# Optimization experiments

Measured on AMD Instinct MI355X. Metric: run time of the kernel, lower is better.

The kernel has to match this reference:

```python
import jax, jax.numpy as jnp
import numpy as np

STRIDES = (8, 16, 32, 64, 128)
LEVEL_HW = ((128, 160), (64, 80), (32, 40), (16, 20), (8, 10))
IMG_H, IMG_W = 1024, 1280
B, NUM_CLASSES = 16, 20
SCORE_THR, IOU_THR, MAX_DET = 0.05, 0.6, 1000


def _coords_all():
    # coords_fmap2orig for every level, concatenated -> [N, 2] (x, y)
    cs = []
    for (h, w), s in zip(LEVEL_HW, STRIDES):
        sx = jnp.arange(w, dtype=jnp.float32) * s + s // 2
        sy = jnp.arange(h, dtype=jnp.float32) * s + s // 2
        yy, xx = jnp.meshgrid(sy, sx, indexing='ij')
        cs.append(jnp.stack([xx.reshape(-1), yy.reshape(-1)], -1))
    return jnp.concatenate(cs, 0)


def _reshape_cat(levels):
    # list of [B,C,h,w] -> [B, sum(h*w), C]
    return jnp.concatenate(
        [p.transpose(0, 2, 3, 1).reshape(p.shape[0], -1, p.shape[1]) for p in levels], 1)


def _decode(cls_l, cnt_l, reg_l, coords):
    cls = jax.nn.sigmoid(_reshape_cat(cls_l))           # [B,N,C]
    cnt = jax.nn.sigmoid(_reshape_cat(cnt_l))[..., 0]   # [B,N]
    reg = _reshape_cat(reg_l)                           # [B,N,4] ltrb
    scores = jnp.sqrt(jnp.max(cls, -1) * cnt)           # add_centerness + sqrt
    classes = jnp.argmax(cls, -1) + 1
    boxes = jnp.concatenate([coords[None] - reg[..., :2], coords[None] + reg[..., 2:]], -1)
    return scores, classes, boxes


def _nms_keep(boxes, scores, classes, valid):
    # masked greedy per-class NMS on fixed size M; returns keep mask [M]
    boxes = jax.lax.stop_gradient(boxes)
    scores = jax.lax.stop_gradient(scores)
    maxc = jnp.max(jnp.where(valid[:, None], boxes, 0.0))
    b = boxes + (classes.astype(boxes.dtype) * (maxc + 1.0))[:, None]  # class offsets
    order = jnp.argsort(-jnp.where(valid, scores, -jnp.inf))
    b = b[order]
    v = valid[order]
    x1, y1, x2, y2 = b[:, 0], b[:, 1], b[:, 2], b[:, 3]
    areas = (x2 - x1 + 1.0) * (y2 - y1 + 1.0)
    iw = jnp.clip(jnp.minimum(x2[:, None], x2[None, :]) - jnp.maximum(x1[:, None], x1[None, :]) + 1.0, 0.0)
    ih = jnp.clip(jnp.minimum(y2[:, None], y2[None, :]) - jnp.maximum(y1[:, None], y1[None, :]) + 1.0, 0.0)
    inter = iw * ih
    iou = inter / (areas[:, None] + areas[None, :] - inter)
    M = boxes.shape[0]

    def body(i, carry):
        keep, sup = carry
        k = v[i] & (~sup[i])
        keep = keep.at[i].set(k)
        sup = sup | (k & (iou[i] > IOU_THR))
        return keep, sup

    keep_s, _ = jax.lax.fori_loop(0, M, body, (jnp.zeros(M, bool), jnp.zeros(M, bool)))
    return jnp.zeros(M, bool).at[order].set(keep_s)


def _forward(args):
    cls_r, cnt_r, reg_r = args[0:5], args[5:10], args[10:15]
    cls_i, cnt_i, reg_i = args[15:20], args[20:25], args[25:30]
    coords = _coords_all()
    s_r, c_r, b_r = _decode(cls_r, cnt_r, reg_r, coords)
    s_i, c_i, b_i = _decode(cls_i, cnt_i, reg_i, coords)
    scores = jnp.concatenate([s_r, s_i], 1)   # [B, 2N]
    classes = jnp.concatenate([c_r, c_i], 1)
    boxes = jnp.concatenate([b_r, b_i], 1)
    top_s, top_i = jax.lax.top_k(scores, MAX_DET)
    top_c = jnp.take_along_axis(classes, top_i, 1)
    top_b = jnp.take_along_axis(boxes, top_i[..., None], 1)
    valid = top_s >= SCORE_THR
    keep = jax.vmap(_nms_keep)(top_b, top_s, top_c, valid)
    # ClipBoxes: clamp to image bounds
    top_b = jnp.maximum(top_b, 0.0)
    xs = jnp.minimum(top_b[..., 0::2], IMG_W - 1.0)
    ys = jnp.minimum(top_b[..., 1::2], IMG_H - 1.0)
    top_b = jnp.stack([xs[..., 0], ys[..., 0], xs[..., 1], ys[..., 1]], -1)
    kf = keep.astype(top_s.dtype)
    return top_s * kf, top_c * keep, top_b * kf[..., None], keep


def setup_inputs() -> dict:
    key = jax.random.key(0)
    chans = {'cls': NUM_CLASSES, 'cnt': 1, 'reg': 4}
    inp = {}
    i = 0
    for mod in ('r', 'i'):
        for kind in ('cls', 'cnt', 'reg'):
            for l, (h, w) in enumerate(LEVEL_HW):
                k = jax.random.fold_in(key, i); i += 1
                inp[f'{kind}_{mod}_{l}'] = jax.random.normal(k, (B, chans[kind], h, w), jnp.float32)
    return inp


def reference(cls_r_0, cls_r_1, cls_r_2, cls_r_3, cls_r_4,
              cnt_r_0, cnt_r_1, cnt_r_2, cnt_r_3, cnt_r_4,
              reg_r_0, reg_r_1, reg_r_2, reg_r_3, reg_r_4,
              cls_i_0, cls_i_1, cls_i_2, cls_i_3, cls_i_4,
              cnt_i_0, cnt_i_1, cnt_i_2, cnt_i_3, cnt_i_4,
              reg_i_0, reg_i_1, reg_i_2, reg_i_3, reg_i_4):
    args = [cls_r_0, cls_r_1, cls_r_2, cls_r_3, cls_r_4,
            cnt_r_0, cnt_r_1, cnt_r_2, cnt_r_3, cnt_r_4,
            reg_r_0, reg_r_1, reg_r_2, reg_r_3, reg_r_4,
            cls_i_0, cls_i_1, cls_i_2, cls_i_3, cls_i_4,
            cnt_i_0, cnt_i_1, cnt_i_2, cnt_i_3, cnt_i_4,
            reg_i_0, reg_i_1, reg_i_2, reg_i_3, reg_i_4]
    return _forward(args)
```

## Files before the change

### kernel.cpp

```cpp
#include <hip/hip_runtime.h>
#include <hip/hip_bf16.h>

typedef unsigned long long u64;
typedef unsigned int u32;

#define NTOT    54560
#define NMOD    27280
#define BATCH   16
#define KPAD    1024
#define MAXD    1000
#define NBIN    16384
#define CAND    6144

struct Ptrs { const float* p[30]; };

constexpr size_t SZ_KEY   = (size_t)BATCH * NTOT * 8;
constexpr size_t SZ_TOPK  = (size_t)BATCH * KPAD * 8;
constexpr size_t SZ_TRAW  = (size_t)BATCH * KPAD * 16;
constexpr size_t SZ_T1    = (size_t)BATCH * KPAD * 4;
constexpr size_t SZ_MAXC  = (size_t)BATCH * 32 * 4;
constexpr size_t SZ_VALID = (size_t)BATCH * 32 * 4;
constexpr size_t SZ_MASK  = (size_t)BATCH * KPAD * 32 * 4;

constexpr size_t OFF_KEY    = 0;
constexpr size_t OFF_TOPK   = OFF_KEY   + SZ_KEY;
constexpr size_t OFF_TRAW   = OFF_TOPK  + SZ_TOPK;
constexpr size_t OFF_TSCORE = OFF_TRAW  + SZ_TRAW;
constexpr size_t OFF_TCLSF  = OFF_TSCORE+ SZ_T1;
constexpr size_t OFF_MAXC   = OFF_TCLSF + SZ_T1;
constexpr size_t OFF_VALID  = OFF_MAXC  + SZ_MAXC;
constexpr size_t OFF_MASK   = OFF_VALID + SZ_VALID;

__device__ inline void level_of(int nm, int& l, int& pos, int& w, int& s, int& hw) {
    if (nm < 20480)      { l = 0; pos = nm;         w = 160; s = 8;   hw = 20480; }
    else if (nm < 25600) { l = 1; pos = nm - 20480; w = 80;  s = 16;  hw = 5120; }
    else if (nm < 26880) { l = 2; pos = nm - 25600; w = 40;  s = 32;  hw = 1280; }
    else if (nm < 27200) { l = 3; pos = nm - 26880; w = 20;  s = 64;  hw = 320; }
    else                 { l = 4; pos = nm - 27200; w = 10;  s = 128; hw = 80; }
}

__device__ inline float sigm(float x) { return 1.0f / (1.0f + expf(-x)); }

__device__ inline void ld_lds16(const float* g, float* l) {
    __builtin_amdgcn_global_load_lds(
        (const __attribute__((address_space(1))) void*)g,
        (__attribute__((address_space(3))) void*)l, 16, 0, 0);
}

__global__ __launch_bounds__(128)
void decode_kernel(Ptrs ptrs, u64* __restrict__ keyAll) {
    __shared__ float lds[21 * 512];
    int cc = blockIdx.x;
    int b = blockIdx.y;

    if (cc >= 100) {
        int t = (cc - 100) * 128 + threadIdx.x;
        if (t >= 3360) return;
        int mod = t / 1680;
        int tm = t % 1680;
        int q = t & 3;
        int nm = 25600 + (tm & ~3);
        int l, pos, w, s, hw;
        level_of(nm, l, pos, w, s, hw);
        (void)w; (void)s;
        const float* clsP = ptrs.p[mod * 15 + l];
        const float* cntP = ptrs.p[mod * 15 + 5 + l];
        const float4* cb = (const float4*)(clsP + (size_t)b * 20 * hw + pos);
        int hw4 = hw >> 2;
        int c0 = q * 5;
        float4 v[5];
        #pragma unroll
        for (int c = 0; c < 5; ++c) v[c] = cb[(size_t)(c0 + c) * hw4];
        float4 cv = *(const float4*)(cntP + (size_t)b * hw + pos);
        float4 mx = v[0];
        #pragma unroll
        for (int c = 1; c < 5; ++c) {
            mx.x = fmaxf(mx.x, v[c].x); mx.y = fmaxf(mx.y, v[c].y);
            mx.z = fmaxf(mx.z, v[c].z); mx.w = fmaxf(mx.w, v[c].w);
        }
        mx.x = fmaxf(mx.x, __shfl_xor(mx.x, 1));
        mx.y = fmaxf(mx.y, __shfl_xor(mx.y, 1));
        mx.z = fmaxf(mx.z, __shfl_xor(mx.z, 1));
        mx.w = fmaxf(mx.w, __shfl_xor(mx.w, 1));
        mx.x = fmaxf(mx.x, __shfl_xor(mx.x, 2));
        mx.y = fmaxf(mx.y, __shfl_xor(mx.y, 2));
        mx.z = fmaxf(mx.z, __shfl_xor(mx.z, 2));
        mx.w = fmaxf(mx.w, __shfl_xor(mx.w, 2));
        float ma = (q & 1) ? ((q & 2) ? mx.w : mx.y) : ((q & 2) ? mx.z : mx.x);
        float ca = (q & 1) ? ((q & 2) ? cv.w : cv.y) : ((q & 2) ? cv.z : cv.x);
        u32 sb = __float_as_uint(sqrtf(__fmul_rn(sigm(ma), sigm(ca))));
        int n = mod * NMOD + nm + q;
        keyAll[(size_t)b * NTOT + n] = ((u64)sb << 16) | (u64)(65535 - n);
        return;
    }

    int mod = cc / 50, c = cc % 50;
    int l     = (c < 40) ? 0 : 1;
    int hw    = (c < 40) ? 20480 : 5120;
    int pos0  = (c < 40) ? c * 512 : (c - 40) * 512;
    int nmb   = (l == 0) ? pos0 : 20480 + pos0;
    const float* clsP = ptrs.p[mod * 15 + l];
    const float* cntP = ptrs.p[mod * 15 + 5 + l];
    int wave = threadIdx.x >> 6, lane = threadIdx.x & 63;

    const float* cbase = clsP + (size_t)b * 20 * hw + pos0 + wave * 256 + lane * 4;
    float* dbase = lds + wave * 256;
    #pragma unroll
    for (int ch = 0; ch < 20; ++ch)
        ld_lds16(cbase + (size_t)ch * hw, dbase + ch * 512);
    ld_lds16(cntP + (size_t)b * hw + pos0 + wave * 256 + lane * 4, dbase + 20 * 512);
    __syncthreads();

    int t = threadIdx.x;
    const float4* l4 = (const float4*)lds;
    float4 mx = l4[t];
    #pragma unroll
    for (int ch = 1; ch < 20; ++ch) {
        float4 v = l4[ch * 128 + t];
        mx.x = fmaxf(mx.x, v.x); mx.y = fmaxf(mx.y, v.y);
        mx.z = fmaxf(mx.z, v.z); mx.w = fmaxf(mx.w, v.w);
    }
    float4 cv = l4[20 * 128 + t];

    int n = mod * NMOD + nmb + t * 4;
    u32 s0 = __float_as_uint(sqrtf(__fmul_rn(sigm(mx.x), sigm(cv.x))));
    u32 s1 = __float_as_uint(sqrtf(__fmul_rn(sigm(mx.y), sigm(cv.y))));
    u32 s2 = __float_as_uint(sqrtf(__fmul_rn(sigm(mx.z), sigm(cv.z))));
    u32 s3 = __float_as_uint(sqrtf(__fmul_rn(sigm(mx.w), sigm(cv.w))));
    ulonglong2* ka2 = (ulonglong2*)(keyAll + (size_t)b * NTOT + n);
    ulonglong2 k01, k23;
    k01.x = ((u64)s0 << 16) | (u64)(65535 - n);
    k01.y = ((u64)s1 << 16) | (u64)(65535 - (n + 1));
    k23.x = ((u64)s2 << 16) | (u64)(65535 - (n + 2));
    k23.y = ((u64)s3 << 16) | (u64)(65535 - (n + 3));
    ka2[0] = k01; ka2[1] = k23;
}

__global__ __launch_bounds__(1024)
void select_kernel(const u64* __restrict__ keyAll, u64* __restrict__ topkey,
                   u32* __restrict__ maxcG) {
    int b = blockIdx.x, tid = threadIdx.x;
    int lane = tid & 63, wid = tid >> 6;
    __shared__ u32 shist[NBIN];
    __shared__ u64 scand[CAND];
    __shared__ u64 stopk[KPAD];
    __shared__ u32 warep[16];
    __shared__ int sB1;

    if (tid == 0) maxcG[b * 32] = 0u;
    #pragma unroll
    for (int j = 0; j < NBIN / 1024; ++j) shist[tid + j * 1024] = 0u;
    __syncthreads();

    const u64* keys = keyAll + (size_t)b * NTOT;
    const u64 SENT = ~0ull;
    for (int n0 = 0; n0 < NTOT; n0 += 8192) {
        u64 kk[8];
        #pragma unroll
        for (int r = 0; r < 8; ++r) {
            int idx = n0 + r * 1024 + tid;
            kk[r] = (idx < NTOT) ? keys[idx] : SENT;
        }
        #pragma unroll
        for (int r = 0; r < 8; ++r)
            if (kk[r] != SENT) atomicAdd(&shist[(u32)(kk[r] >> 32)], 1u);
    }
    __syncthreads();

    u32 loc[16]; u32 sum = 0;
    #pragma unroll
    for (int j = 0; j < 16; ++j) { loc[j] = shist[NBIN - 1 - (tid * 16 + j)]; sum += loc[j]; }
    u32 v = sum;
    #pragma unroll
    for (int off = 1; off < 64; off <<= 1) {
        u32 t2 = (u32)__shfl_up((int)v, off);
        if (lane >= off) v += t2;
    }
    if (lane == 63) warep[wid] = v;
    __syncthreads();
    if (tid < 16) {
        u32 p = warep[tid];
        #pragma unroll
        for (int off = 1; off < 16; off <<= 1) {
            u32 t2 = (u32)__shfl_up((int)p, off);
            if (tid >= off) p += t2;
        }
        warep[tid] = p;
    }
    __syncthreads();
    u32 incl = v + (wid ? warep[wid - 1] : 0u);
    u32 excl = incl - sum;
    if (excl < (u32)MAXD && incl >= (u32)MAXD) {
        u32 c = excl;
        #pragma unroll
        for (int j = 0; j < 16; ++j) {
            c += loc[j];
            if (c >= (u32)MAXD) { sB1 = NBIN - 1 - (tid * 16 + j); break; }
        }
    }
    u32 run = excl;
    #pragma unroll
    for (int j = 0; j < 16; ++j) {
        int bin = NBIN - 1 - (tid * 16 + j);
        shist[bin] = run;
        run += loc[j];
    }
    __syncthreads();
    int B1 = sB1;

    for (int n0 = 0; n0 < NTOT; n0 += 8192) {
        u64 kk[8];
        #pragma unroll
        for (int r = 0; r < 8; ++r) {
            int idx = n0 + r * 1024 + tid;
            kk[r] = (idx < NTOT) ? keys[idx] : 0ull;
        }
        #pragma unroll
        for (int r = 0; r < 8; ++r) {
            if (kk[r] != 0ull && (int)(kk[r] >> 32) >= B1) {
                u32 p = atomicAdd(&shist[(u32)(kk[r] >> 32)], 1u);
                if (p < CAND) scand[p] = kk[r];
            }
        }
    }
    __syncthreads();
    int Ctot = min((int)shist[B1], CAND);

    for (int i = tid; i < Ctot; i += 1024) {
        u64 ki = scand[i];
        int bin = (int)(ki >> 32);
        int st = (int)shist[bin + 1];
        int en = min((int)shist[bin], Ctot);
        int pos = st;
        for (int j = st; j < en; ++j) pos += (scand[j] > ki) ? 1 : 0;
        if (pos < MAXD) stopk[pos] = ki;
    }
    __syncthreads();
    if (tid < MAXD) topkey[(size_t)b * KPAD + tid] = stopk[tid];
}

__global__ __launch_bounds__(128)
void gather_kernel(Ptrs ptrs, const u64* __restrict__ topkey,
                   float4* __restrict__ traw, float* __restrict__ tscore,
                   float* __restrict__ tclsf, u32* __restrict__ validwords,
                   u32* __restrict__ maxcG) {
    #pragma clang fp contract(off)
    int b = blockIdx.y;
    int tid = threadIdx.x;
    int half = tid & 1;
    int i = blockIdx.x * 64 + (tid >> 1);
    int active = (i < MAXD);

    float score = 0.f;
    float best = -1.0f; int bi = 0;
    float ra = 0.f, rb2 = 0.f;
    int pos = 0, w = 1, s = 0;
    if (active) {
        u64 key = topkey[(size_t)b * KPAD + i];
        int n = 65535 - (int)(key & 0xFFFFull);
        score = __uint_as_float((u32)(key >> 16));
        int mod = (n >= NMOD) ? 1 : 0;
        int nm = n - mod * NMOD;
        int l, hw;
        level_of(nm, l, pos, w, s, hw);
        const float* clsP = ptrs.p[mod * 15 + l];
        const float* regP = ptrs.p[mod * 15 + 10 + l];
        const float* cbp = clsP + (size_t)b * 20 * hw + pos;
        const float* rbp = regP + (size_t)b * 4 * hw + pos;
        float cl[10];
        int c0 = half * 10;
        #pragma unroll
        for (int c = 0; c < 10; ++c) cl[c] = cbp[(size_t)(c0 + c) * hw];
        ra  = rbp[(size_t)(half * 2) * hw];
        rb2 = rbp[(size_t)(half * 2 + 1) * hw];
        #pragma unroll
        for (int c = 0; c < 10; ++c) {
            float p = sigm(cl[c]);
            if (p > best) { best = p; bi = c0 + c; }
        }
    }
    float po  = __shfl_xor(best, 1);
    int   bio = __shfl_xor(bi, 1);
    float rao = __shfl_xor(ra, 1);
    float rbo = __shfl_xor(rb2, 1);
    if (half == 0) { if (po > best)  { best = po; bi = bio; } }
    else           { if (po >= best) { best = po; bi = bio; } }
    float clsf = active ? (float)(bi + 1) : 0.f;
    float r0 = half ? rao : ra,  r1 = half ? rbo : rb2;
    float r2 = half ? ra  : rao, r3 = half ? rb2 : rbo;

    float4 bx = make_float4(0.f, 0.f, 0.f, 0.f);
    if (active) {
        int xi = pos % w, yi = pos / w;
        float cx = (float)(xi * s + (s >> 1));
        float cy = (float)(yi * s + (s >> 1));
        bx.x = cx - r0; bx.y = cy - r1; bx.z = cx + r2; bx.w = cy + r3;
    }
    int valid = active && (score >= 0.05f) && (half == 0);
    float contrib = valid ? fmaxf(0.0f, fmaxf(fmaxf(bx.x, bx.y), fmaxf(bx.z, bx.w))) : 0.0f;
    float red = contrib;
    #pragma unroll
    for (int off = 32; off > 0; off >>= 1) red = fmaxf(red, __shfl_down(red, off));
    if ((tid & 63) == 0) atomicMax(&maxcG[b * 32], __float_as_uint(red));
    u64 ball = __ballot(valid != 0);
    if ((tid & 63) == 0) {
        u32 word = 0;
        for (int j = 0; j < 32; ++j) word |= (u32)((ball >> (2 * j)) & 1ull) << j;
        validwords[b * 32 + blockIdx.x * 2 + (tid >> 6)] = word;
    }
    if (half == 0) {
        size_t oo = (size_t)b * KPAD + i;
        traw[oo] = bx; tscore[oo] = score; tclsf[oo] = clsf;
    }
}

#define SW(t) ((((t) & 31) << 3) | ((t) >> 5))
__global__ __launch_bounds__(256)
void mask_kernel(const float4* __restrict__ traw, const float* __restrict__ tclsf,
                 const u32* __restrict__ maxcG, u32* __restrict__ maskG) {
    #pragma clang fp contract(off)
    int u = blockIdx.x, b = blockIdx.y, tid = threadIdx.x;
    int g, wg;
    if (u < 32)      { g = u >> 2;              wg = u & 3; }
    else if (u < 56) { int d = u - 32; g = 8  + d / 3;        wg = 1 + d % 3; }
    else if (u < 72) { int d = u - 56; g = 16 + (d >> 1);     wg = 2 + (d & 1); }
    else             { g = 24 + (u - 72);       wg = 3; }
    int i0 = g * 32, j0 = wg * 256;
    float m1 = __uint_as_float(maxcG[b * 32]) + 1.0f;

    __shared__ float cx1[256], cy1[256], cx2[256], cy2[256], ca[256];
    {
        int t = tid;
        float4 f = traw[(size_t)b * KPAD + j0 + t];
        float o = __fmul_rn(tclsf[(size_t)b * KPAD + j0 + t], m1);
        float ox1 = __fadd_rn(f.x, o), oy1 = __fadd_rn(f.y, o);
        float ox2 = __fadd_rn(f.z, o), oy2 = __fadd_rn(f.w, o);
        float dw = ox2 - ox1 + 1.0f;
        float dh = oy2 - oy1 + 1.0f;
        int ts = SW(t);
        cx1[ts] = ox1; cy1[ts] = oy1; cx2[ts] = ox2; cy2[ts] = oy2;
        ca[ts] = __fmul_rn(dw, dh);
    }
    __syncthreads();

    int ir = tid >> 3, wr = tid & 7;
    int i = i0 + ir;
    float4 fi = traw[(size_t)b * KPAD + i];
    float oi = __fmul_rn(tclsf[(size_t)b * KPAD + i], m1);
    float ix1 = __fadd_rn(fi.x, oi), iy1 = __fadd_rn(fi.y, oi);
    float ix2 = __fadd_rn(fi.z, oi), iy2 = __fadd_rn(fi.w, oi);
    float dwi = ix2 - ix1 + 1.0f, dhi = iy2 - iy1 + 1.0f;
    float ai = __fmul_rn(dwi, dhi);
    u32 bits = 0;
    int jb = wr * 32;
    for (int jj = 0; jj < 32; ++jj) {
        int js = SW(jb + jj);
        float iw = fminf(ix2, cx2[js]) - fmaxf(ix1, cx1[js]) + 1.0f;
        iw = fmaxf(iw, 0.0f);
        float ih = fminf(iy2, cy2[js]) - fmaxf(iy1, cy1[js]) + 1.0f;
        ih = fmaxf(ih, 0.0f);
        float inter = iw * ih;
        float denom = (ai + ca[js]) - inter;
        float iou = inter / denom;
        bits |= (iou > 0.6f) ? (1u << jj) : 0u;
    }
    maskG[((size_t)b * KPAD + i) * 32 + wg * 8 + wr] = bits;
}

__global__ __launch_bounds__(512)
void scan_out_kernel(const u32* __restrict__ maskG, const u32* __restrict__ validbits,
                     const float4* __restrict__ traw, const float* __restrict__ tscore,
                     const float* __restrict__ tclsf, float* __restrict__ out) {
    __shared__ u32 sm[KPAD * 32];
    __shared__ u32 keeps[32];
    int b = blockIdx.x, tid = threadIdx.x;

    const uint4* s4 = (const uint4*)(maskG + (size_t)b * KPAD * 32);
    uint4* d4 = (uint4*)sm;
    #pragma unroll
    for (int r = 0; r < 16; ++r) {
        int w4 = tid + r * 512;
        int row = w4 >> 3, c4 = w4 & 7;
        d4[(row << 3) | (c4 ^ (row & 7))] = s4[w4];
    }
    __syncthreads();

    if (tid < 64) {
        int lane = tid, lw = lane & 31;
        int rbase = (lane >> 5) << 4;
        u32 vword = validbits[b * 32 + lw];
        u32 removed = 0u, keepw = 0u;
        for (int g = 0; g < 32; ++g) {
            int i0 = g << 5;
            u32 intra = sm[((i0 + lw) << 5) | (g ^ ((lw & 7) << 2))];
            u32 remg = (u32)__builtin_amdgcn_readlane((int)removed, g);
            u32 valg = (u32)__builtin_amdgcn_readlane((int)vword, g);
            u32 cand = valg & ~remg;
            u32 keep32 = 0u, sup = 0u;
            #pragma unroll
            for (int i = 0; i < 32; ++i) {
                u32 mi = (u32)__builtin_amdgcn_readlane((int)intra, i);
                u32 kb = cand & ~sup & (1u << i);
                sup |= kb ? mi : 0u;
                keep32 |= kb;
            }
            u32 ksh = keep32 >> rbase;
            u32 acc0 = 0u, acc1 = 0u;
            #pragma unroll
            for (int r = 0; r < 16; r += 2) {
                u32 r0 = sm[((i0 + rbase + r)     << 5) | (lw ^ ((r & 7) << 2))];
                u32 r1 = sm[((i0 + rbase + r + 1) << 5) | (lw ^ (((r + 1) & 7) << 2))];
                acc0 |= ((ksh >> r) & 1u)       ? r0 : 0u;
                acc1 |= ((ksh >> (r + 1)) & 1u) ? r1 : 0u;
            }
            u32 acc = acc0 | acc1;
            acc |= (u32)__shfl_xor((int)acc, 32);
            removed |= acc;
            if (lw == g) keepw = keep32;
        }
        if (lane < 32) keeps[lw] = keepw;
    }
    __syncthreads();

    const int BQ = BATCH * MAXD;
    for (int s2 = tid; s2 < MAXD; s2 += 512) {
        u32 kf = (keeps[s2 >> 5] >> (s2 & 31)) & 1u;
        size_t oo = (size_t)b * KPAD + s2;
        float score = tscore[oo];
        float clsf = tclsf[oo];
        float4 bx = traw[oo];
        float x1 = fminf(fmaxf(bx.x, 0.f), 1279.f);
        float y1 = fminf(fmaxf(bx.y, 0.f), 1023.f);
        float x2 = fminf(fmaxf(bx.z, 0.f), 1279.f);
        float y2 = fminf(fmaxf(bx.w, 0.f), 1023.f);
        int base = b * MAXD + s2;
        out[base] = kf ? score : 0.0f;
        out[BQ + base] = kf ? clsf : 0.0f;
        float* ob = out + 2 * BQ + (size_t)base * 4;
        ob[0] = kf ? x1 : 0.f; ob[1] = kf ? y1 : 0.f;
        ob[2] = kf ? x2 : 0.f; ob[3] = kf ? y2 : 0.f;
        out[6 * BQ + base] = kf ? 1.0f : 0.0f;
    }
}

extern "C" void kernel_launch(void* const* d_in, const int* in_sizes, int n_in,
                              void* d_out, int out_size, void* d_ws, size_t ws_size,
                              hipStream_t stream) {
    Ptrs ptrs;
    for (int i = 0; i < 30; ++i) ptrs.p[i] = (const float*)d_in[i];

    char* ws = (char*)d_ws;
    u64*    keyAll    = (u64*)   (ws + OFF_KEY);
    u64*    topkey    = (u64*)   (ws + OFF_TOPK);
    float4* traw      = (float4*)(ws + OFF_TRAW);
    float*  tscore    = (float*) (ws + OFF_TSCORE);
    float*  tclsf     = (float*) (ws + OFF_TCLSF);
    u32*    maxcG     = (u32*)   (ws + OFF_MAXC);
    u32*    validbits = (u32*)   (ws + OFF_VALID);
    u32*    maskG     = (u32*)   (ws + OFF_MASK);
    float*  out       = (float*)d_out;

    decode_kernel<<<dim3(127, BATCH), 128, 0, stream>>>(ptrs, keyAll);
    select_kernel<<<BATCH, 1024, 0, stream>>>(keyAll, topkey, maxcG);
    gather_kernel<<<dim3(16, BATCH), 128, 0, stream>>>(ptrs, topkey, traw, tscore, tclsf,
                                                       validbits, maxcG);
    mask_kernel<<<dim3(80, BATCH), 256, 0, stream>>>(traw, tclsf, maxcG, maskG);
    scan_out_kernel<<<BATCH, 512, 0, stream>>>(maskG, validbits, traw, tscore, tclsf, out);
}
```

Measured before the change: 236.3 us.

## Split top-k select into global histogram, scan, scatter and fixup kernels

The single-block-per-image select kernel is replaced by a pipeline. The histogram is built with global atomics inside the decode kernel, which removes one full pass over the keys. A scan kernel then finds the threshold bin, a multi-block scatter kernel writes candidates to global memory, and a fixup kernel ranks them in LDS. This spreads the select work over more CUs than the old 16 blocks. The cost is contended global atomics, extra kernel launches and a zeroing kernel.

```diff
diff --git a/kernel.cpp b/kernel.cpp
--- a/kernel.cpp
+++ b/kernel.cpp
@@ -21,6 +21,9 @@
 constexpr size_t SZ_MAXC  = (size_t)BATCH * 32 * 4;
 constexpr size_t SZ_VALID = (size_t)BATCH * 32 * 4;
 constexpr size_t SZ_MASK  = (size_t)BATCH * KPAD * 32 * 4;
+constexpr size_t SZ_GHIST = (size_t)BATCH * NBIN * 4;
+constexpr size_t SZ_GB1   = 256;
+constexpr size_t SZ_GCAND = (size_t)BATCH * CAND * 8;
 
 constexpr size_t OFF_KEY    = 0;
 constexpr size_t OFF_TOPK   = OFF_KEY   + SZ_KEY;
@@ -30,6 +33,9 @@
 constexpr size_t OFF_MAXC   = OFF_TCLSF + SZ_T1;
 constexpr size_t OFF_VALID  = OFF_MAXC  + SZ_MAXC;
 constexpr size_t OFF_MASK   = OFF_VALID + SZ_VALID;
+constexpr size_t OFF_GHIST  = OFF_MASK  + SZ_MASK;
+constexpr size_t OFF_GB1    = OFF_GHIST + SZ_GHIST;
+constexpr size_t OFF_GCAND  = OFF_GB1   + SZ_GB1;
 
 __device__ inline void level_of(int nm, int& l, int& pos, int& w, int& s, int& hw) {
     if (nm < 20480)      { l = 0; pos = nm;         w = 160; s = 8;   hw = 20480; }
@@ -47,11 +53,19 @@
         (__attribute__((address_space(3))) void*)l, 16, 0, 0);
 }
 
+__global__ __launch_bounds__(256)
+void init_kernel(uint4* __restrict__ ghist4, u32* __restrict__ maxcG) {
+    int i = blockIdx.x * 256 + threadIdx.x;
+    ghist4[i] = make_uint4(0u, 0u, 0u, 0u);
+    if (i < BATCH) maxcG[i * 32] = 0u;
+}
+
 __global__ __launch_bounds__(128)
-void decode_kernel(Ptrs ptrs, u64* __restrict__ keyAll) {
+void decode_kernel(Ptrs ptrs, u64* __restrict__ keyAll, u32* __restrict__ ghist) {
     __shared__ float lds[21 * 512];
     int cc = blockIdx.x;
     int b = blockIdx.y;
+    u32* gh = ghist + (size_t)b * NBIN;
 
     if (cc >= 100) {
         int t = (cc - 100) * 128 + threadIdx.x;
@@ -91,6 +105,7 @@
         u32 sb = __float_as_uint(sqrtf(__fmul_rn(sigm(ma), sigm(ca))));
         int n = mod * NMOD + nm + q;
         keyAll[(size_t)b * NTOT + n] = ((u64)sb << 16) | (u64)(65535 - n);
+        atomicAdd(&gh[sb >> 16], 1u);
         return;
     }
 
@@ -134,42 +149,23 @@
     k23.x = ((u64)s2 << 16) | (u64)(65535 - (n + 2));
     k23.y = ((u64)s3 << 16) | (u64)(65535 - (n + 3));
     ka2[0] = k01; ka2[1] = k23;
+    atomicAdd(&gh[s0 >> 16], 1u);
+    atomicAdd(&gh[s1 >> 16], 1u);
+    atomicAdd(&gh[s2 >> 16], 1u);
+    atomicAdd(&gh[s3 >> 16], 1u);
 }
 
 __global__ __launch_bounds__(1024)
-void select_kernel(const u64* __restrict__ keyAll, u64* __restrict__ topkey,
-                   u32* __restrict__ maxcG) {
+void scan_kernel(u32* __restrict__ ghist, int* __restrict__ gB1) {
     int b = blockIdx.x, tid = threadIdx.x;
     int lane = tid & 63, wid = tid >> 6;
-    __shared__ u32 shist[NBIN];
-    __shared__ u64 scand[CAND];
-    __shared__ u64 stopk[KPAD];
     __shared__ u32 warep[16];
     __shared__ int sB1;
-
-    if (tid == 0) maxcG[b * 32] = 0u;
-    #pragma unroll
-    for (int j = 0; j < NBIN / 1024; ++j) shist[tid + j * 1024] = 0u;
-    __syncthreads();
-
-    const u64* keys = keyAll + (size_t)b * NTOT;
-    const u64 SENT = ~0ull;
-    for (int n0 = 0; n0 < NTOT; n0 += 8192) {
-        u64 kk[8];
-        #pragma unroll
-        for (int r = 0; r < 8; ++r) {
-            int idx = n0 + r * 1024 + tid;
-            kk[r] = (idx < NTOT) ? keys[idx] : SENT;
-        }
-        #pragma unroll
-        for (int r = 0; r < 8; ++r)
-            if (kk[r] != SENT) atomicAdd(&shist[(u32)(kk[r] >> 32)], 1u);
-    }
-    __syncthreads();
+    u32* gh = ghist + (size_t)b * NBIN;
 
     u32 loc[16]; u32 sum = 0;
     #pragma unroll
-    for (int j = 0; j < 16; ++j) { loc[j] = shist[NBIN - 1 - (tid * 16 + j)]; sum += loc[j]; }
+    for (int j = 0; j < 16; ++j) { loc[j] = gh[NBIN - 1 - (tid * 16 + j)]; sum += loc[j]; }
     u32 v = sum;
     #pragma unroll
     for (int off = 1; off < 64; off <<= 1) {
@@ -202,35 +198,53 @@
     #pragma unroll
     for (int j = 0; j < 16; ++j) {
         int bin = NBIN - 1 - (tid * 16 + j);
-        shist[bin] = run;
+        gh[bin] = run;
         run += loc[j];
     }
     __syncthreads();
-    int B1 = sB1;
-
-    for (int n0 = 0; n0 < NTOT; n0 += 8192) {
-        u64 kk[8];
-        #pragma unroll
-        for (int r = 0; r < 8; ++r) {
-            int idx = n0 + r * 1024 + tid;
-            kk[r] = (idx < NTOT) ? keys[idx] : 0ull;
-        }
-        #pragma unroll
-        for (int r = 0; r < 8; ++r) {
-            if (kk[r] != 0ull && (int)(kk[r] >> 32) >= B1) {
-                u32 p = atomicAdd(&shist[(u32)(kk[r] >> 32)], 1u);
-                if (p < CAND) scand[p] = kk[r];
-            }
-        }
-    }
-    __syncthreads();
-    int Ctot = min((int)shist[B1], CAND);
-
+    if (tid == 0) gB1[b] = sB1;
+}
+
+__global__ __launch_bounds__(1024)
+void scatter_kernel(const u64* __restrict__ keyAll, u32* __restrict__ ghist,
+                    const int* __restrict__ gB1, u64* __restrict__ gcand) {
+    int b = blockIdx.y, tid = threadIdx.x;
+    int n0 = blockIdx.x * 8192;
+    int B1 = gB1[b];
+    const u64* keys = keyAll + (size_t)b * NTOT;
+    u32* gh = ghist + (size_t)b * NBIN;
+    u64* gc = gcand + (size_t)b * CAND;
+    u64 kk[8];
+    #pragma unroll
+    for (int r = 0; r < 8; ++r) {
+        int idx = n0 + r * 1024 + tid;
+        kk[r] = (idx < NTOT) ? keys[idx] : 0ull;
+    }
+    #pragma unroll
+    for (int r = 0; r < 8; ++r) {
+        if (kk[r] != 0ull && (int)(kk[r] >> 32) >= B1) {
+            u32 p = atomicAdd(&gh[(u32)(kk[r] >> 32)], 1u);
+            if (p < CAND) gc[p] = kk[r];
+        }
+    }
+}
+
+__global__ __launch_bounds__(1024)
+void fixup_kernel(const u64* __restrict__ gcand, const u32* __restrict__ ghist,
+                  const int* __restrict__ gB1, u64* __restrict__ topkey) {
+    __shared__ u64 scand[CAND];
+    __shared__ u64 stopk[KPAD];
+    int b = blockIdx.x, tid = threadIdx.x;
+    const u32* gh = ghist + (size_t)b * NBIN;
+    int B1 = gB1[b];
+    int Ctot = min((int)gh[B1], CAND);
+    for (int i = tid; i < Ctot; i += 1024) scand[i] = gcand[(size_t)b * CAND + i];
+    __syncthreads();
     for (int i = tid; i < Ctot; i += 1024) {
         u64 ki = scand[i];
         int bin = (int)(ki >> 32);
-        int st = (int)shist[bin + 1];
-        int en = min((int)shist[bin], Ctot);
+        int st = (int)gh[bin + 1];
+        int en = min((int)gh[bin], Ctot);
         int pos = st;
         for (int j = st; j < en; ++j) pos += (scand[j] > ki) ? 1 : 0;
         if (pos < MAXD) stopk[pos] = ki;
@@ -458,10 +472,16 @@
     u32*    maxcG     = (u32*)   (ws + OFF_MAXC);
     u32*    validbits = (u32*)   (ws + OFF_VALID);
     u32*    maskG     = (u32*)   (ws + OFF_MASK);
+    u32*    ghist     = (u32*)   (ws + OFF_GHIST);
+    int*    gB1       = (int*)   (ws + OFF_GB1);
+    u64*    gcand     = (u64*)   (ws + OFF_GCAND);
     float*  out       = (float*)d_out;
 
-    decode_kernel<<<dim3(127, BATCH), 128, 0, stream>>>(ptrs, keyAll);
-    select_kernel<<<BATCH, 1024, 0, stream>>>(keyAll, topkey, maxcG);
+    init_kernel<<<256, 256, 0, stream>>>((uint4*)ghist, maxcG);
+    decode_kernel<<<dim3(127, BATCH), 128, 0, stream>>>(ptrs, keyAll, ghist);
+    scan_kernel<<<BATCH, 1024, 0, stream>>>(ghist, gB1);
+    scatter_kernel<<<dim3(7, BATCH), 1024, 0, stream>>>(keyAll, ghist, gB1, gcand);
+    fixup_kernel<<<BATCH, 1024, 0, stream>>>(gcand, ghist, gB1, topkey);
     gather_kernel<<<dim3(16, BATCH), 128, 0, stream>>>(ptrs, topkey, traw, tscore, tclsf,
                                                        validbits, maxcG);
     mask_kernel<<<dim3(80, BATCH), 256, 0, stream>>>(traw, tclsf, maxcG, maskG);
```

Measured after the change: 335.7 us. 1.42x slower.
